# Optimization experiments

Hardware: AMD Instinct MI355X
Metric: run time of the kernel (lower is better)

The kernel has to match this reference:

```python
import jax, jax.numpy as jnp
import numpy as np

NTOKENS = 8192
H = 1024
FFN = 2048
NEXPERTS = 64
TOPK = 2
M = NTOKENS * TOPK  # total routed slots


def setup_inputs() -> dict:
    key = jax.random.key(0)
    k1, k2, k3 = jax.random.split(key, 3)
    inputs_shard = jax.random.normal(k1, (NTOKENS, H), dtype=jnp.float32)
    w1 = jax.random.normal(k2, (NEXPERTS, H, FFN), dtype=jnp.float32) * 0.02
    w2 = jax.random.normal(k3, (NEXPERTS, FFN, H), dtype=jnp.float32) * 0.02
    # Balanced routing: each expert receives exactly M // NEXPERTS slots.
    rng = np.random.default_rng(0)
    per_expert = M // NEXPERTS
    eid_flat = rng.permutation(np.repeat(np.arange(M // per_expert), per_expert))  # [M] expert id per (token,k)
    order = np.argsort(eid_flat, kind='stable')  # slot -> flat (token,k) index
    scatter_flat = np.empty(M, dtype=np.int64)
    scatter_flat[order] = np.arange(M)  # (token,k) -> slot in expert-sorted buffer
    scatter_index = jnp.asarray(scatter_flat.reshape(NTOKENS, TOPK))
    splits = jnp.full((NEXPERTS,), per_expert, dtype=jnp.int64)
    return {"inputs_shard": inputs_shard, "w1": w1, "w2": w2,
            "scatter_index": scatter_index, "splits": splits}


def reference(inputs_shard, w1, w2, scatter_index, splits):
    ntokens, topk = scatter_index.shape
    m = ntokens * topk
    nexperts = w1.shape[0]
    per_expert = m // nexperts  # splits are balanced by construction
    # AG-scatter: place each token copy into its expert-sorted slot.
    slot_to_tk = jnp.argsort(scatter_index.reshape(-1))  # slot -> (token,k) flat idx
    token = slot_to_tk // topk                            # slot -> source token
    expanded = inputs_shard[token]                        # [M, H]
    # Grouped GEMM 1 (h -> ffn) + exact gelu, per expert block.
    xg = expanded.reshape(nexperts, per_expert, -1)       # [G, M/G, H]
    h1 = jnp.einsum('geh,ghf->gef', xg, w1)               # [G, M/G, FFN]
    a = jax.nn.gelu(h1, approximate=False)
    # Grouped GEMM 2 (ffn -> h).
    h2 = jnp.einsum('gef,gfh->geh', a, w2).reshape(m, -1)  # [M, H]
    # Gather-RS: gather topk partials per token and reduce (sum).
    out = h2[scatter_index.reshape(-1)].reshape(ntokens, topk, -1).sum(axis=1)
    return out
```

## Files before the change

kernel.cpp:

```cpp
#include <hip/hip_runtime.h>
#include <hip/hip_bf16.h>
#include <math.h>

#define NTOK 8192
#define HD   1024
#define FFND 2048
#define NE   64
#define MTOT 16384
#define PER_E 256

typedef __attribute__((ext_vector_type(8))) short bh8;
typedef __attribute__((ext_vector_type(4))) float f4;
typedef unsigned short u16;
typedef unsigned int   u32;

__device__ __forceinline__ u16 f2bf(float f) {
  union { float f; u32 u; } x; x.f = f;
  u32 r = x.u + 0x7fffu + ((x.u >> 16) & 1u);
  return (u16)(r >> 16);
}

__device__ __forceinline__ float bf2f(u16 b) {
  union { u32 u; float f; } x; x.u = ((u32)b) << 16; return x.f;
}

__device__ __forceinline__ u32 pk2(float lo, float hi) {
  __hip_bfloat162 h = __float22bfloat162_rn(make_float2(lo, hi));
  union { __hip_bfloat162 h; u32 u; } c; c.h = h;
  return c.u;
}

__global__ void k_build_s2t(const int* __restrict__ sidx, int* __restrict__ s2t) {
  int i = blockIdx.x * 256 + threadIdx.x;
  s2t[sidx[i]] = i >> 1;
}

__global__ void k_gather_x(const float* __restrict__ inp, const int* __restrict__ s2t,
                           u16* __restrict__ X) {
  for (int idx = blockIdx.x * 256 + threadIdx.x; idx < MTOT * (HD / 8);
       idx += 2048 * 256) {
    int slot = idx >> 7;
    int c    = idx & 127;
    const float* src = inp + (size_t)s2t[slot] * HD + c * 8;
    float v[8];
    *(f4*)(v)     = *(const f4*)(src);
    *(f4*)(v + 4) = *(const f4*)(src + 4);
    u32 o[4];
    #pragma unroll
    for (int j = 0; j < 4; ++j) o[j] = pk2(v[2 * j], v[2 * j + 1]);
    *(uint4*)(X + (size_t)slot * HD + c * 8) = *(uint4*)o;
  }
}

template<int K, int N, bool GELU>
__global__ __launch_bounds__(512, 2)
void moe_gemm(const u16* __restrict__ Abf, const float* __restrict__ Bf,
              u16* __restrict__ outp)
{
  constexpr int BM = 256, BN = 256, BK = 64;
  constexpr int NB = N / BN;
  constexpr int NT = K / BK;
  constexpr int NF = 8;
  constexpr int ABYTES = BM * 128;
  __shared__ __align__(16) char lds[2 * ABYTES + BN * 128];
  char* Bs = lds + 2 * ABYTES;

  const int d = blockIdx.y * NB + blockIdx.x;
  const int x = d & 7, j = d >> 3;
  const int e  = x * (NE / 8) + j / NB;
  const int n0 = (j % NB) * BN;
  const int row0 = e * PER_E;
  const int tid  = threadIdx.x;
  const int lane = tid & 63, wid = tid >> 6;
  const int wr   = wid >> 1, wc = wid & 1;

  const u16*   Arow = Abf + (size_t)row0 * K;
  const float* Bsrc = Bf + (size_t)e * K * N + n0;

  const int nq = (tid & 63) * 4;
  const int kg = tid >> 6;

  auto stageA = [&](int buf, int k0) {
    char* dst = lds + buf * ABYTES;
    #pragma unroll
    for (int i = 0; i < 4; ++i) {
      int c = i * 512 + tid;
      int r = c >> 3, kc = c & 7;
      int kswz = kc ^ (r & 7);
      __builtin_amdgcn_global_load_lds(
          (const void*)(Arow + (size_t)r * K + k0 + kswz * 8),
          (void*)(dst + c * 16), 16, 0, 0);
    }
  };
  auto loadB = [&](f4* br4, int k0) {
    #pragma unroll
    for (int jj = 0; jj < 8; ++jj)
      br4[jj] = __builtin_nontemporal_load(
          (const f4*)(Bsrc + (size_t)(k0 + kg * 8 + jj) * N + nq));
  };
  auto writeB = [&](const f4* br4) {
    #pragma unroll
    for (int i = 0; i < 4; ++i) {
      int n = nq + i;
      u32 q[4];
      #pragma unroll
      for (int jj = 0; jj < 4; ++jj)
        q[jj] = pk2(br4[2 * jj][i], br4[2 * jj + 1][i]);
      *(uint4*)(Bs + n * 128 + ((kg * 16) ^ ((n & 7) << 4))) = *(uint4*)q;
    }
  };

  f4 acc[4][NF] = {};
  f4 breg[8];

  loadB(breg, 0);
  __builtin_amdgcn_sched_barrier(0);
  stageA(0, 0);
  asm volatile("s_waitcnt vmcnt(4)" ::: "memory");
  __builtin_amdgcn_sched_barrier(0);
  writeB(breg);
  asm volatile("s_waitcnt lgkmcnt(0)" ::: "memory");
  __builtin_amdgcn_sched_barrier(0);
  __builtin_amdgcn_s_barrier();
  __builtin_amdgcn_sched_barrier(0);

  int cur = 0;
  for (int t = 0; t < NT; ++t) {
    const char* As = lds + cur * ABYTES;
    if (t + 1 < NT) {
      loadB(breg, (t + 1) * BK);
      __builtin_amdgcn_sched_barrier(0);
      stageA(cur ^ 1, (t + 1) * BK);
      asm volatile("s_waitcnt vmcnt(12)" ::: "memory");
    } else {
      asm volatile("s_waitcnt vmcnt(0)" ::: "memory");
    }
    __builtin_amdgcn_sched_barrier(0);
    __builtin_amdgcn_s_setprio(1);
    #pragma unroll
    for (int kk = 0; kk < 2; ++kk) {
      int kByte = kk * 64 + ((lane >> 4) << 4);
      bh8 a[4], b[NF];
      #pragma unroll
      for (int m = 0; m < 4; ++m) {
        int r = wr * 64 + m * 16 + (lane & 15);
        a[m] = *(const bh8*)(As + r * 128 + (kByte ^ ((r & 7) << 4)));
      }
      #pragma unroll
      for (int n = 0; n < NF; ++n) {
        int r = wc * 128 + n * 16 + (lane & 15);
        b[n] = *(const bh8*)(Bs + r * 128 + (kByte ^ ((r & 7) << 4)));
      }
      #pragma unroll
      for (int m = 0; m < 4; ++m)
        #pragma unroll
        for (int n = 0; n < NF; ++n)
          acc[m][n] = __builtin_amdgcn_mfma_f32_16x16x32_bf16(a[m], b[n], acc[m][n], 0, 0, 0);
    }
    __builtin_amdgcn_s_setprio(0);
    __builtin_amdgcn_s_barrier();
    __builtin_amdgcn_sched_barrier(0);
    if (t + 1 < NT) {
      asm volatile("s_waitcnt vmcnt(4)" ::: "memory");
      __builtin_amdgcn_sched_barrier(0);
      writeB(breg);
      asm volatile("s_waitcnt lgkmcnt(0)" ::: "memory");
      __builtin_amdgcn_sched_barrier(0);
      __builtin_amdgcn_s_barrier();
      __builtin_amdgcn_sched_barrier(0);
      cur ^= 1;
    }
  }

  #pragma unroll
  for (int m = 0; m < 4; ++m) {
    #pragma unroll
    for (int n = 0; n < NF; ++n) {
      int rowb = wr * 64 + m * 16 + ((lane >> 4) << 2);
      int col  = n0 + wc * 128 + n * 16 + (lane & 15);
      #pragma unroll
      for (int jj = 0; jj < 4; ++jj) {
        float xv = acc[m][n][jj];
        if (GELU) {
          float y = fminf(fmaxf(xv, -8.f), 8.f);
          float u = 0.7978845608f * (y + 0.044715f * y * y * y);
          float t2 = __expf(-2.f * u);
          float g = __fdividef(y, 1.f + t2);
          outp[(size_t)(row0 + rowb + jj) * N + col] = f2bf(g);
        } else {
          outp[(size_t)(row0 + rowb + jj) * N + col] = f2bf(xv);
        }
      }
    }
  }
}

__global__ void k_reduce(const u16* __restrict__ h2, const int* __restrict__ sidx,
                         float* __restrict__ out) {
  for (int i = blockIdx.x * 256 + threadIdx.x; i < NTOK * (HD / 4);
       i += 2048 * 256) {
    int t = i >> 8, c = i & 255;
    const u16* r0 = h2 + (size_t)sidx[2 * t] * HD + c * 4;
    const u16* r1 = h2 + (size_t)sidx[2 * t + 1] * HD + c * 4;
    u16 a0[4], a1[4];
    *(uint2*)a0 = *(const uint2*)r0;
    *(uint2*)a1 = *(const uint2*)r1;
    f4 s;
    #pragma unroll
    for (int jj = 0; jj < 4; ++jj) s[jj] = bf2f(a0[jj]) + bf2f(a1[jj]);
    *(f4*)(out + (size_t)t * HD + c * 4) = s;
  }
}

extern "C" void kernel_launch(void* const* d_in, const int* in_sizes, int n_in,
                              void* d_out, int out_size, void* d_ws, size_t ws_size,
                              hipStream_t stream) {
  const float* inp  = (const float*)d_in[0];
  const float* w1   = (const float*)d_in[1];
  const float* w2   = (const float*)d_in[2];
  const int*   sidx = (const int*)d_in[3];
  float* out = (float*)d_out;

  char* ws   = (char*)d_ws;
  int*   s2t = (int*)ws;
  u16*   X   = (u16*)(ws + (1 << 20));
  u16*   act = (u16*)(ws + (1 << 20) + (32u << 20));
  u16*   h2  = (u16*)(ws + (1 << 20) + (96u << 20));

  k_build_s2t<<<MTOT / 256, 256, 0, stream>>>(sidx, s2t);
  k_gather_x<<<2048, 256, 0, stream>>>(inp, s2t, X);
  moe_gemm<HD, FFND, true><<<dim3(FFND / 256, NE), 512, 0, stream>>>(X, w1, act);
  moe_gemm<FFND, HD, false><<<dim3(HD / 256, NE), 512, 0, stream>>>(act, w2, h2);
  k_reduce<<<2048, 256, 0, stream>>>(h2, sidx, out);
}
```

Measured before the change: 273.7 us.

## Fuse token gather and bf16 conversion into first grouped GEMM A-loading

```diff
diff --git a/kernel.cpp b/kernel.cpp
--- a/kernel.cpp
+++ b/kernel.cpp
@@ -14,6 +14,8 @@
 typedef unsigned short u16;
 typedef unsigned int   u32;
 
+#define SB0 __builtin_amdgcn_sched_barrier(0)
+
 __device__ __forceinline__ u16 f2bf(float f) {
   union { float f; u32 u; } x; x.f = f;
   u32 r = x.u + 0x7fffu + ((x.u >> 16) & 1u);
@@ -35,27 +37,152 @@
   s2t[sidx[i]] = i >> 1;
 }
 
-__global__ void k_gather_x(const float* __restrict__ inp, const int* __restrict__ s2t,
-                           u16* __restrict__ X) {
-  for (int idx = blockIdx.x * 256 + threadIdx.x; idx < MTOT * (HD / 8);
-       idx += 2048 * 256) {
-    int slot = idx >> 7;
-    int c    = idx & 127;
-    const float* src = inp + (size_t)s2t[slot] * HD + c * 8;
-    float v[8];
-    *(f4*)(v)     = *(const f4*)(src);
-    *(f4*)(v + 4) = *(const f4*)(src + 4);
-    u32 o[4];
-    #pragma unroll
-    for (int j = 0; j < 4; ++j) o[j] = pk2(v[2 * j], v[2 * j + 1]);
-    *(uint4*)(X + (size_t)slot * HD + c * 8) = *(uint4*)o;
-  }
-}
-
-template<int K, int N, bool GELU>
+template<int K, int N>
 __global__ __launch_bounds__(512, 2)
-void moe_gemm(const u16* __restrict__ Abf, const float* __restrict__ Bf,
-              u16* __restrict__ outp)
+void moe_gemm1(const float* __restrict__ inp, const int* __restrict__ s2t,
+               const float* __restrict__ Bf, u16* __restrict__ actout)
+{
+  constexpr int BM = 256, BN = 256, BK = 64;
+  constexpr int NB = N / BN;
+  constexpr int NT = K / BK;
+  constexpr int NF = 8;
+  constexpr int ABYTES = BM * 128;
+  __shared__ __align__(16) char lds[ABYTES + BN * 128];
+  char* Bs = lds + ABYTES;
+
+  const int d = blockIdx.y * NB + blockIdx.x;
+  const int x = d & 7, j = d >> 3;
+  const int e  = x * (NE / 8) + j / NB;
+  const int n0 = (j % NB) * BN;
+  const int row0 = e * PER_E;
+  const int tid  = threadIdx.x;
+  const int lane = tid & 63, wid = tid >> 6;
+  const int wr   = wid >> 1, wc = wid & 1;
+
+  const float* Bsrc = Bf + (size_t)e * K * N + n0;
+  const int nq = (tid & 63) * 4;
+  const int kg = tid >> 6;
+
+  int arow[4]; const float* asrc[4];
+  #pragma unroll
+  for (int i = 0; i < 4; ++i) {
+    int c = i * 512 + tid;
+    arow[i] = c >> 3;
+    asrc[i] = inp + (size_t)s2t[row0 + arow[i]] * K;
+  }
+
+  auto loadA = [&](f4* ar, int k0) {
+    #pragma unroll
+    for (int i = 0; i < 4; ++i) {
+      int c = i * 512 + tid;
+      int kc = c & 7, r = arow[i];
+      int kswz = kc ^ (r & 7);
+      const float* p = asrc[i] + k0 + kswz * 8;
+      ar[i * 2]     = *(const f4*)(p);
+      ar[i * 2 + 1] = *(const f4*)(p + 4);
+    }
+  };
+  auto writeA = [&](const f4* ar) {
+    #pragma unroll
+    for (int i = 0; i < 4; ++i) {
+      int c = i * 512 + tid;
+      u32 q[4];
+      q[0] = pk2(ar[i * 2][0],     ar[i * 2][1]);
+      q[1] = pk2(ar[i * 2][2],     ar[i * 2][3]);
+      q[2] = pk2(ar[i * 2 + 1][0], ar[i * 2 + 1][1]);
+      q[3] = pk2(ar[i * 2 + 1][2], ar[i * 2 + 1][3]);
+      *(uint4*)(lds + c * 16) = *(uint4*)q;
+    }
+  };
+  auto loadB = [&](f4* br4, int k0) {
+    #pragma unroll
+    for (int jj = 0; jj < 8; ++jj)
+      br4[jj] = __builtin_nontemporal_load(
+          (const f4*)(Bsrc + (size_t)(k0 + kg * 8 + jj) * N + nq));
+  };
+  auto writeB = [&](const f4* br4) {
+    #pragma unroll
+    for (int i = 0; i < 4; ++i) {
+      int n = nq + i;
+      u32 q[4];
+      #pragma unroll
+      for (int jj = 0; jj < 4; ++jj)
+        q[jj] = pk2(br4[2 * jj][i], br4[2 * jj + 1][i]);
+      *(uint4*)(Bs + n * 128 + ((kg * 16) ^ ((n & 7) << 4))) = *(uint4*)q;
+    }
+  };
+
+  f4 acc[4][NF] = {};
+  f4 breg[8], areg[8];
+
+  loadB(breg, 0); SB0;
+  loadA(areg, 0); SB0;
+  asm volatile("s_waitcnt vmcnt(0)" ::: "memory"); SB0;
+  writeB(breg);
+  writeA(areg);
+  asm volatile("s_waitcnt lgkmcnt(0)" ::: "memory"); SB0;
+  __builtin_amdgcn_s_barrier(); SB0;
+
+  for (int t = 0; t < NT; ++t) {
+    if (t + 1 < NT) {
+      loadB(breg, (t + 1) * BK); SB0;
+      loadA(areg, (t + 1) * BK); SB0;
+    }
+    __builtin_amdgcn_s_setprio(1);
+    #pragma unroll
+    for (int kk = 0; kk < 2; ++kk) {
+      int kByte = kk * 64 + ((lane >> 4) << 4);
+      bh8 a[4], b[NF];
+      #pragma unroll
+      for (int m = 0; m < 4; ++m) {
+        int r = wr * 64 + m * 16 + (lane & 15);
+        a[m] = *(const bh8*)(lds + r * 128 + (kByte ^ ((r & 7) << 4)));
+      }
+      #pragma unroll
+      for (int n = 0; n < NF; ++n) {
+        int r = wc * 128 + n * 16 + (lane & 15);
+        b[n] = *(const bh8*)(Bs + r * 128 + (kByte ^ ((r & 7) << 4)));
+      }
+      #pragma unroll
+      for (int m = 0; m < 4; ++m)
+        #pragma unroll
+        for (int n = 0; n < NF; ++n)
+          acc[m][n] = __builtin_amdgcn_mfma_f32_16x16x32_bf16(a[m], b[n], acc[m][n], 0, 0, 0);
+    }
+    __builtin_amdgcn_s_setprio(0);
+    __builtin_amdgcn_s_barrier(); SB0;
+    if (t + 1 < NT) {
+      asm volatile("s_waitcnt vmcnt(0)" ::: "memory"); SB0;
+      writeB(breg);
+      writeA(areg);
+      asm volatile("s_waitcnt lgkmcnt(0)" ::: "memory"); SB0;
+      __builtin_amdgcn_s_barrier(); SB0;
+    }
+  }
+
+  #pragma unroll
+  for (int m = 0; m < 4; ++m) {
+    #pragma unroll
+    for (int n = 0; n < NF; ++n) {
+      int rowb = wr * 64 + m * 16 + ((lane >> 4) << 2);
+      int col  = n0 + wc * 128 + n * 16 + (lane & 15);
+      #pragma unroll
+      for (int jj = 0; jj < 4; ++jj) {
+        float xv = acc[m][n][jj];
+        float y = fminf(fmaxf(xv, -8.f), 8.f);
+        float u = 0.7978845608f * (y + 0.044715f * y * y * y);
+        float t2 = __expf(-2.f * u);
+        float g = __fdividef(y, 1.f + t2);
+        actout[(size_t)(row0 + rowb + jj) * N + col] = f2bf(g);
+      }
+    }
+  }
+}
+
+template<int K, int N>
+__global__ __launch_bounds__(512, 2)
+void moe_gemm2(const u16* __restrict__ Abf, const float* __restrict__ Bf,
+               u16* __restrict__ outp)
 {
   constexpr int BM = 256, BN = 256, BK = 64;
   constexpr int NB = N / BN;
@@ -76,7 +203,6 @@
 
   const u16*   Arow = Abf + (size_t)row0 * K;
   const float* Bsrc = Bf + (size_t)e * K * N + n0;
-
   const int nq = (tid & 63) * 4;
   const int kg = tid >> 6;
 
@@ -113,29 +239,24 @@
   f4 acc[4][NF] = {};
   f4 breg[8];
 
-  loadB(breg, 0);
-  __builtin_amdgcn_sched_barrier(0);
+  loadB(breg, 0); SB0;
   stageA(0, 0);
-  asm volatile("s_waitcnt vmcnt(4)" ::: "memory");
-  __builtin_amdgcn_sched_barrier(0);
+  asm volatile("s_waitcnt vmcnt(4)" ::: "memory"); SB0;
   writeB(breg);
-  asm volatile("s_waitcnt lgkmcnt(0)" ::: "memory");
-  __builtin_amdgcn_sched_barrier(0);
-  __builtin_amdgcn_s_barrier();
-  __builtin_amdgcn_sched_barrier(0);
+  asm volatile("s_waitcnt lgkmcnt(0)" ::: "memory"); SB0;
+  __builtin_amdgcn_s_barrier(); SB0;
 
   int cur = 0;
   for (int t = 0; t < NT; ++t) {
     const char* As = lds + cur * ABYTES;
     if (t + 1 < NT) {
-      loadB(breg, (t + 1) * BK);
-      __builtin_amdgcn_sched_barrier(0);
+      loadB(breg, (t + 1) * BK); SB0;
       stageA(cur ^ 1, (t + 1) * BK);
       asm volatile("s_waitcnt vmcnt(12)" ::: "memory");
     } else {
       asm volatile("s_waitcnt vmcnt(0)" ::: "memory");
     }
-    __builtin_amdgcn_sched_barrier(0);
+    SB0;
     __builtin_amdgcn_s_setprio(1);
     #pragma unroll
     for (int kk = 0; kk < 2; ++kk) {
@@ -158,16 +279,12 @@
           acc[m][n] = __builtin_amdgcn_mfma_f32_16x16x32_bf16(a[m], b[n], acc[m][n], 0, 0, 0);
     }
     __builtin_amdgcn_s_setprio(0);
-    __builtin_amdgcn_s_barrier();
-    __builtin_amdgcn_sched_barrier(0);
+    __builtin_amdgcn_s_barrier(); SB0;
     if (t + 1 < NT) {
-      asm volatile("s_waitcnt vmcnt(4)" ::: "memory");
-      __builtin_amdgcn_sched_barrier(0);
+      asm volatile("s_waitcnt vmcnt(4)" ::: "memory"); SB0;
       writeB(breg);
-      asm volatile("s_waitcnt lgkmcnt(0)" ::: "memory");
-      __builtin_amdgcn_sched_barrier(0);
-      __builtin_amdgcn_s_barrier();
-      __builtin_amdgcn_sched_barrier(0);
+      asm volatile("s_waitcnt lgkmcnt(0)" ::: "memory"); SB0;
+      __builtin_amdgcn_s_barrier(); SB0;
       cur ^= 1;
     }
   }
@@ -179,18 +296,8 @@
       int rowb = wr * 64 + m * 16 + ((lane >> 4) << 2);
       int col  = n0 + wc * 128 + n * 16 + (lane & 15);
       #pragma unroll
-      for (int jj = 0; jj < 4; ++jj) {
-        float xv = acc[m][n][jj];
-        if (GELU) {
-          float y = fminf(fmaxf(xv, -8.f), 8.f);
-          float u = 0.7978845608f * (y + 0.044715f * y * y * y);
-          float t2 = __expf(-2.f * u);
-          float g = __fdividef(y, 1.f + t2);
-          outp[(size_t)(row0 + rowb + jj) * N + col] = f2bf(g);
-        } else {
-          outp[(size_t)(row0 + rowb + jj) * N + col] = f2bf(xv);
-        }
-      }
+      for (int jj = 0; jj < 4; ++jj)
+        outp[(size_t)(row0 + rowb + jj) * N + col] = f2bf(acc[m][n][jj]);
     }
   }
 }
@@ -223,13 +330,11 @@
 
   char* ws   = (char*)d_ws;
   int*   s2t = (int*)ws;
-  u16*   X   = (u16*)(ws + (1 << 20));
   u16*   act = (u16*)(ws + (1 << 20) + (32u << 20));
   u16*   h2  = (u16*)(ws + (1 << 20) + (96u << 20));
 
   k_build_s2t<<<MTOT / 256, 256, 0, stream>>>(sidx, s2t);
-  k_gather_x<<<2048, 256, 0, stream>>>(inp, s2t, X);
-  moe_gemm<HD, FFND, true><<<dim3(FFND / 256, NE), 512, 0, stream>>>(X, w1, act);
-  moe_gemm<FFND, HD, false><<<dim3(HD / 256, NE), 512, 0, stream>>>(act, w2, h2);
+  moe_gemm1<HD, FFND><<<dim3(FFND / 256, NE), 512, 0, stream>>>(inp, s2t, w1, act);
+  moe_gemm2<FFND, HD><<<dim3(HD / 256, NE), 512, 0, stream>>>(act, w2, h2);
   k_reduce<<<2048, 256, 0, stream>>>(h2, sidx, out);
 }
```

Result: no change. 269.3 us (-1.6%).
